# Performance work log

Hardware: AMD Instinct MI355X
Metric: run time of the kernel (lower is better)

## Reference

```python
import jax, jax.numpy as jnp
import numpy as np

N_NODES = 50000
N_EDGES = 800000
IN_DIM = 128
HID = 128
N_LAYERS = 3
MASK_RATE = 0.3
NUM_MASK = int(MASK_RATE * N_NODES)  # 15000


def setup_inputs() -> dict:
    key = jax.random.key(0)
    ks = jax.random.split(key, 8)
    attr = jax.random.normal(ks[0], (N_NODES, IN_DIM), dtype=jnp.float32)
    src = jax.random.randint(ks[1], (N_EDGES,), 0, N_NODES, dtype=jnp.int32)
    dst = jax.random.randint(ks[2], (N_EDGES,), 0, N_NODES, dtype=jnp.int32)
    # GraphConv weights (glorot-ish scale)
    Ws = jax.random.normal(ks[3], (N_LAYERS, HID, HID), dtype=jnp.float32) * (1.0 / np.sqrt(HID))
    bs = jnp.zeros((N_LAYERS, HID), dtype=jnp.float32)
    dec_W = jax.random.normal(ks[4], (HID, IN_DIM), dtype=jnp.float32) * (1.0 / np.sqrt(HID))
    dec_b = jnp.zeros((IN_DIM,), dtype=jnp.float32)
    mask_token = jnp.zeros((1, IN_DIM), dtype=jnp.float32)
    # torch.randperm(N)[:num_mask]
    perm = jax.random.permutation(ks[5], N_NODES)
    mask_nodes = perm[:NUM_MASK].astype(jnp.int32)
    return {"attr": attr, "src": src, "dst": dst, "Ws": Ws, "bs": bs,
            "dec_W": dec_W, "dec_b": dec_b, "mask_token": mask_token,
            "mask_nodes": mask_nodes}


def reference(attr, src, dst, Ws, bs, dec_W, dec_b, mask_token, mask_nodes):
    # degree norms (DGL GraphConv norm='both'), zero-degree clamped to 1
    ones = jnp.ones((src.shape[0],), dtype=jnp.float32)
    out_deg = jax.ops.segment_sum(ones, src, num_segments=N_NODES)
    in_deg = jax.ops.segment_sum(ones, dst, num_segments=N_NODES)
    norm_src = jnp.power(jnp.clip(out_deg, 1.0, None), -0.5)[:, None]  # [N,1]
    norm_dst = jnp.power(jnp.clip(in_deg, 1.0, None), -0.5)[:, None]

    # mask node features with the mask token
    h = attr.at[mask_nodes].set(mask_token[0])

    for i in range(N_LAYERS):
        h = h @ Ws[i]                       # [N, H]
        m = (h * norm_src)[src]             # gather: [E, H]
        agg = jax.ops.segment_sum(m, dst, num_segments=N_NODES)
        h = jax.nn.relu(agg * norm_dst + bs[i])

    recon = h @ dec_W + dec_b               # [N, IN_DIM]
    x_orig = attr[mask_nodes]
    x_rec = recon[mask_nodes]
    loss = jnp.mean((x_rec - x_orig) ** 2)
    return loss
```

## Files before the change

### kernel.cpp

```cpp
#include <hip/hip_runtime.h>
#include <hip/hip_fp16.h>

#define HID 128
#define NN 50000
#define NW4 (NN / 4)
#define NB 256
#define CST 64

typedef _Float16 f16;
typedef f16 f16x8 __attribute__((ext_vector_type(8)));
typedef float f32x4 __attribute__((ext_vector_type(4)));

__device__ __forceinline__ unsigned char enc8(float v) {
  __half h = __float2half(v);
  unsigned short b;
  __builtin_memcpy(&b, &h, 2);
  return (unsigned char)((b + 0x80u) >> 8);
}
__device__ __forceinline__ __half2 dec8h2(unsigned v) {
  unsigned p = __builtin_amdgcn_perm(0u, v, 0x01040004u);
  __half2 h2;
  __builtin_memcpy(&h2, &p, 4);
  return h2;
}
__device__ __forceinline__ f16x8 dec8x8(const unsigned char* p) {
  uint2 u = *(const uint2*)p;
  unsigned r[4];
  r[0] = __builtin_amdgcn_perm(0u, u.x, 0x01040004u);
  r[1] = __builtin_amdgcn_perm(0u, u.x, 0x03040204u);
  r[2] = __builtin_amdgcn_perm(0u, u.y, 0x01040004u);
  r[3] = __builtin_amdgcn_perm(0u, u.y, 0x03040204u);
  f16x8 out;
  __builtin_memcpy(&out, r, 16);
  return out;
}

__global__ __launch_bounds__(256) void hist_kernel(
    const int* __restrict__ src, const int* __restrict__ dst,
    unsigned* __restrict__ pin, unsigned* __restrict__ pout,
    unsigned char* __restrict__ rank, float* __restrict__ d_out_f,
    unsigned* __restrict__ mmap_w, int E, int chunk) {
  __shared__ unsigned hist[NW4];
  const int b = blockIdx.x;
  const int e0 = b * chunk, e1 = min(E, e0 + chunk);
  if (b == 0 && threadIdx.x == 0) *d_out_f = 0.f;
  if (b < 49) {
    int wi = b * 256 + threadIdx.x;
    if (wi < NW4) mmap_w[wi] = 0;
  }

  for (int i = threadIdx.x; i < NW4; i += 256) hist[i] = 0;
  __syncthreads();
  for (int e = e0 + threadIdx.x; e < e1; e += 256) {
    int d = dst[e];
    unsigned sh = 8u * (d & 3);
    unsigned old = atomicAdd(&hist[d >> 2], 1u << sh);
    rank[e] = (unsigned char)((old >> sh) & 0xffu);
  }
  __syncthreads();
  unsigned* rowI = pin + (size_t)b * NW4;
  for (int i = threadIdx.x; i < NW4; i += 256) rowI[i] = hist[i];
  __syncthreads();
  for (int i = threadIdx.x; i < NW4; i += 256) hist[i] = 0;
  __syncthreads();
  for (int e = e0 + threadIdx.x; e < e1; e += 256) {
    int s = src[e];
    atomicAdd(&hist[s >> 2], 1u << (8u * (s & 3)));
  }
  __syncthreads();
  unsigned* rowO = pout + (size_t)b * NW4;
  for (int i = threadIdx.x; i < NW4; i += 256) rowO[i] = hist[i];
}

__global__ __launch_bounds__(256) void merge_kernel(
    unsigned* __restrict__ pin, const unsigned* __restrict__ pout,
    int* __restrict__ in_cnt, float* __restrict__ ns, float* __restrict__ nd,
    const int* __restrict__ mask, unsigned char* __restrict__ mmap, int nm) {
  int gi = blockIdx.x * 256 + threadIdx.x;
  if (gi < nm) mmap[mask[gi]] = 1;

  __shared__ unsigned tsum[8][32];
  __shared__ unsigned osum[8][32];
  const int wl = threadIdx.x & 31;
  const int tile = threadIdx.x >> 5;
  const int w = blockIdx.x * 32 + wl;
  const bool ok = w < NW4;

  unsigned v[32];
  unsigned s = 0, so = 0;
  if (ok) {
#pragma unroll
    for (int j = 0; j < 32; ++j)
      v[j] = pin[(size_t)(tile * 32 + j) * NW4 + w];
#pragma unroll
    for (int j = 0; j < 32; ++j) {
      unsigned x = v[j];
      v[j] = s;
      s += x;
    }
#pragma unroll
    for (int j = 0; j < 32; ++j)
      so += pout[(size_t)(tile * 32 + j) * NW4 + w];
  }
  tsum[tile][wl] = s;
  osum[tile][wl] = so;
  __syncthreads();
  unsigned toff = 0;
  for (int k = 0; k < tile; ++k) toff += tsum[k][wl];
  if (ok) {
#pragma unroll
    for (int j = 0; j < 32; ++j)
      pin[(size_t)(tile * 32 + j) * NW4 + w] = v[j] + toff;
    if (tile == 7) {
      unsigned tin = toff + s;
      unsigned tout = 0;
#pragma unroll
      for (int k = 0; k < 8; ++k) tout += osum[k][wl];
      int i0 = tin & 0xffu, i1 = (tin >> 8) & 0xffu,
          i2 = (tin >> 16) & 0xffu, i3 = (tin >> 24) & 0xffu;
      int o0 = tout & 0xffu, o1 = (tout >> 8) & 0xffu,
          o2 = (tout >> 16) & 0xffu, o3 = (tout >> 24) & 0xffu;
      ((int4*)in_cnt)[w] = make_int4(i0, i1, i2, i3);
      ((float4*)nd)[w] = make_float4(rsqrtf((float)max(i0, 1)),
                                     rsqrtf((float)max(i1, 1)),
                                     rsqrtf((float)max(i2, 1)),
                                     rsqrtf((float)max(i3, 1)));
      ((float4*)ns)[w] = make_float4(rsqrtf((float)max(o0, 1)),
                                     rsqrtf((float)max(o1, 1)),
                                     rsqrtf((float)max(o2, 1)),
                                     rsqrtf((float)max(o3, 1)));
    }
  }
}

__global__ __launch_bounds__(256) void fillprep_kernel(
    const int* __restrict__ src, const int* __restrict__ dst,
    const unsigned char* __restrict__ rank, const unsigned* __restrict__ pin,
    int* __restrict__ csr,
    const float* __restrict__ attr, const float* __restrict__ Ws,
    const float* __restrict__ decW, const float* __restrict__ ns,
    const float* __restrict__ token, const unsigned char* __restrict__ mmap,
    unsigned char* __restrict__ X, f16* __restrict__ Wt,
    int E, int chunk, int n4) {
  const int b = blockIdx.x;
  if (b < 256) {
    const int e0 = b * chunk, e1 = min(E, e0 + chunk);
    const unsigned* __restrict__ row = pin + (size_t)b * NW4;
    for (int e = e0 + threadIdx.x; e < e1; e += 256) {
      int s = src[e], d = dst[e];
      unsigned base = (row[d >> 2] >> (8u * (d & 3))) & 0xffu;
      csr[d * CST + (int)base + (int)rank[e]] = s;
    }
  } else if (b < 512) {
    int i = (b - 256) * 256 + threadIdx.x;
    int m = i >> 14, rem = i & 16383, n = rem >> 7, k = rem & 127;
    const float* Wsrc = (m < 3) ? (Ws + (size_t)m * 16384) : decW;
    Wt[i] = (f16)Wsrc[k * 128 + n];
  } else {
    int i = (b - 512) * 256 + threadIdx.x;
    if (i < n4) {
      int r = i >> 5, c4 = i & 31;
      float s = ns[r];
      float4 v = mmap[r] ? ((const float4*)token)[c4] : ((const float4*)attr)[i];
      ((uchar4*)X)[i] = make_uchar4(enc8(s * v.x), enc8(s * v.y),
                                    enc8(s * v.z), enc8(s * v.w));
    }
  }
}

__global__ __launch_bounds__(256) void agg_kernel(
    const unsigned short* __restrict__ X, const int* __restrict__ csr,
    const int* __restrict__ in_cnt, const float* __restrict__ nd,
    const int* __restrict__ glist, unsigned short* __restrict__ Y, int n) {
  int ni = (blockIdx.x * blockDim.x + threadIdx.x) >> 6;
  int lane = threadIdx.x & 63;
  if (ni >= n) return;
  int node = glist ? glist[ni] : ni;
  int cnt = in_cnt[node];
  int idx = csr[node * CST + lane];
  __half2 z = __floats2half2_rn(0.f, 0.f);
  __half2 a0 = z, a1 = z, a2 = z, a3 = z;
  int i = 0;
  for (; i + 4 <= cnt; i += 4) {
    int s0 = __shfl(idx, i + 0);
    int s1 = __shfl(idx, i + 1);
    int s2 = __shfl(idx, i + 2);
    int s3 = __shfl(idx, i + 3);
    __half2 v0 = dec8h2(X[(size_t)s0 * 64 + lane]);
    __half2 v1 = dec8h2(X[(size_t)s1 * 64 + lane]);
    __half2 v2 = dec8h2(X[(size_t)s2 * 64 + lane]);
    __half2 v3 = dec8h2(X[(size_t)s3 * 64 + lane]);
    a0 = __hadd2(a0, v0);
    a1 = __hadd2(a1, v1);
    a2 = __hadd2(a2, v2);
    a3 = __hadd2(a3, v3);
  }
  for (; i < cnt; ++i) {
    int s = __shfl(idx, i);
    a0 = __hadd2(a0, dec8h2(X[(size_t)s * 64 + lane]));
  }
  __half2 hs = __hadd2(__hadd2(a0, a1), __hadd2(a2, a3));
  float2 f = __half22float2(hs);
  float ndv = nd[node];
  unsigned char lo = enc8(f.x * ndv), hi = enc8(f.y * ndv);
  Y[(size_t)ni * 64 + lane] = (unsigned short)(lo | (hi << 8));
}

__global__ __launch_bounds__(256) void gemm_layer_kernel(
    const unsigned char* __restrict__ A8, const f16* __restrict__ Wt,
    unsigned char* __restrict__ out, const float* __restrict__ col_bias,
    const float* __restrict__ row_scale, int M) {
  __shared__ f16 Bs[128 * 136];
  const int t = threadIdx.x;
  for (int i = t; i < 2048; i += 256) {
    int n = i >> 4, c = i & 15;
    *(f16x8*)&Bs[n * 136 + c * 8] = *(const f16x8*)&Wt[n * 128 + c * 8];
  }
  const int wave = t >> 6, lane = t & 63;
  const int ln = lane & 15, kq = lane >> 4;
  const int mBase = blockIdx.x * 64 + wave * 16;

  const int am = mBase + ln;
  const int rowA = (am < M) ? am : 0;
  const unsigned char* Ap = A8 + (size_t)rowA * HID + kq * 8;
  f16x8 af[4];
#pragma unroll
  for (int ki = 0; ki < 4; ++ki) af[ki] = dec8x8(Ap + ki * 32);

  f32x4 acc[8];
#pragma unroll
  for (int nt = 0; nt < 8; ++nt) acc[nt] = (f32x4){0.f, 0.f, 0.f, 0.f};
  __syncthreads();
#pragma unroll
  for (int ki = 0; ki < 4; ++ki) {
#pragma unroll
    for (int nt = 0; nt < 8; ++nt) {
      f16x8 bf = *(const f16x8*)&Bs[(nt * 16 + ln) * 136 + ki * 32 + kq * 8];
      acc[nt] = __builtin_amdgcn_mfma_f32_16x16x32_f16(af[ki], bf, acc[nt], 0, 0, 0);
    }
  }
  const int orow = mBase + kq * 4;
  float rs[4];
#pragma unroll
  for (int r = 0; r < 4; ++r)
    rs[r] = (row_scale && orow + r < M) ? row_scale[orow + r] : 1.f;
#pragma unroll
  for (int nt = 0; nt < 8; ++nt) {
    int col = nt * 16 + ln;
    float bb = col_bias[col];
#pragma unroll
    for (int r = 0; r < 4; ++r) {
      int gr = orow + r;
      if (gr < M) {
        float v = fmaxf(acc[nt][r] + bb, 0.f) * rs[r];
        out[(size_t)gr * HID + col] = enc8(v);
      }
    }
  }
}

__global__ __launch_bounds__(256) void gemm_loss_kernel(
    const unsigned char* __restrict__ A8, const f16* __restrict__ Wt,
    const float* __restrict__ col_bias, const int* __restrict__ mask,
    const float* __restrict__ attr, float* __restrict__ out, int M, float scale) {
  __shared__ f16 Bs[128 * 136];
  const int t = threadIdx.x;
  for (int i = t; i < 2048; i += 256) {
    int n = i >> 4, c = i & 15;
    *(f16x8*)&Bs[n * 136 + c * 8] = *(const f16x8*)&Wt[n * 128 + c * 8];
  }
  const int wave = t >> 6, lane = t & 63;
  const int ln = lane & 15, kq = lane >> 4;
  const int mBase = blockIdx.x * 64 + wave * 16;

  const int am = mBase + ln;
  const int rowA = (am < M) ? am : 0;
  const unsigned char* Ap = A8 + (size_t)rowA * HID + kq * 8;
  f16x8 af[4];
#pragma unroll
  for (int ki = 0; ki < 4; ++ki) af[ki] = dec8x8(Ap + ki * 32);

  f32x4 acc[8];
#pragma unroll
  for (int nt = 0; nt < 8; ++nt) acc[nt] = (f32x4){0.f, 0.f, 0.f, 0.f};
  __syncthreads();
#pragma unroll
  for (int ki = 0; ki < 4; ++ki) {
#pragma unroll
    for (int nt = 0; nt < 8; ++nt) {
      f16x8 bf = *(const f16x8*)&Bs[(nt * 16 + ln) * 136 + ki * 32 + kq * 8];
      acc[nt] = __builtin_amdgcn_mfma_f32_16x16x32_f16(af[ki], bf, acc[nt], 0, 0, 0);
    }
  }
  const int orow = mBase + kq * 4;
  int mrow[4];
#pragma unroll
  for (int r = 0; r < 4; ++r) mrow[r] = (orow + r < M) ? mask[orow + r] : -1;
  float part = 0.f;
#pragma unroll
  for (int nt = 0; nt < 8; ++nt) {
    int col = nt * 16 + ln;
    float bb = col_bias[col];
#pragma unroll
    for (int r = 0; r < 4; ++r) {
      if (mrow[r] >= 0) {
        float d = acc[nt][r] + bb - attr[(size_t)mrow[r] * HID + col];
        part += d * d;
      }
    }
  }
#pragma unroll
  for (int off = 32; off > 0; off >>= 1) part += __shfl_down(part, off);
  __shared__ float wsum[4];
  if (lane == 0) wsum[wave] = part;
  __syncthreads();
  if (t == 0)
    atomicAdd(out, (wsum[0] + wsum[1] + wsum[2] + wsum[3]) * scale);
}

extern "C" void kernel_launch(void* const* d_in, const int* in_sizes, int n_in,
                              void* d_out, int out_size, void* d_ws, size_t ws_size,
                              hipStream_t stream) {
  const float* attr  = (const float*)d_in[0];
  const int*   src   = (const int*)d_in[1];
  const int*   dst   = (const int*)d_in[2];
  const float* Ws    = (const float*)d_in[3];
  const float* bs    = (const float*)d_in[4];
  const float* decW  = (const float*)d_in[5];
  const float* decb  = (const float*)d_in[6];
  const float* token = (const float*)d_in[7];
  const int*   mask  = (const int*)d_in[8];

  const int N  = in_sizes[0] / HID;
  const int E  = in_sizes[1];
  const int NM = in_sizes[8];
  const int chunk = (E + NB - 1) / NB;

  char* w = (char*)d_ws;
  unsigned char* X = (unsigned char*)w;  w += (size_t)N * HID;
  unsigned char* Y = (unsigned char*)w;  w += (size_t)N * HID;
  f16* Wt = (f16*)w;           w += (size_t)4 * HID * HID * 2;
  int* csr = (int*)w;          w += (size_t)NN * CST * 4;
  unsigned char* rank = (unsigned char*)w;  w += (size_t)E;
  unsigned* pin = (unsigned*)w;  w += (size_t)NB * NW4 * 4;
  unsigned* pout = (unsigned*)w; w += (size_t)NB * NW4 * 4;
  int* in_cnt = (int*)w;       w += (size_t)N * 4;
  float* ns = (float*)w;       w += (size_t)N * 4;
  float* nd = (float*)w;       w += (size_t)N * 4;
  unsigned char* mmap = (unsigned char*)w;  w += (size_t)NW4 * 4;

  hist_kernel<<<NB, 256, 0, stream>>>(src, dst, pin, pout, rank,
                                      (float*)d_out, (unsigned*)mmap, E, chunk);
  merge_kernel<<<(NW4 + 31) / 32, 256, 0, stream>>>(pin, pout, in_cnt, ns, nd,
                                                    mask, mmap, NM);

  int prep_blocks = 512 + (N * 32 + 255) / 256;
  fillprep_kernel<<<prep_blocks, 256, 0, stream>>>(
      src, dst, rank, pin, csr, attr, Ws, decW, ns, token, mmap,
      X, Wt, E, chunk, N * 32);

  for (int l = 0; l < 2; ++l) {
    agg_kernel<<<(N + 3) / 4, 256, 0, stream>>>(
        (const unsigned short*)X, csr, in_cnt, nd, nullptr,
        (unsigned short*)Y, N);
    gemm_layer_kernel<<<(N + 63) / 64, 256, 0, stream>>>(
        Y, Wt + (size_t)l * HID * HID, X, bs + (size_t)l * HID, ns, N);
  }

  agg_kernel<<<(NM + 3) / 4, 256, 0, stream>>>(
      (const unsigned short*)X, csr, in_cnt, nd, mask,
      (unsigned short*)Y, NM);
  gemm_layer_kernel<<<(NM + 63) / 64, 256, 0, stream>>>(
      Y, Wt + (size_t)2 * HID * HID, X, bs + (size_t)2 * HID, nullptr, NM);

  gemm_loss_kernel<<<(NM + 63) / 64, 256, 0, stream>>>(
      X, Wt + (size_t)3 * HID * HID, decb, mask, attr, (float*)d_out,
      NM, 1.f / ((float)NM * HID));
}
```

Before: 239.5 us.

## Replace deterministic histogram CSR build with global atomic bucket fill

Replaces the three-kernel build (per-block shared-memory histograms, a prefix-merge kernel, and a separate fill pass) with one edge-parallel kernel. It uses global atomics on the in-degree counters to claim CSR slots and atomics on out-degree, and zeroes the counters with a memset. Degree norms are no longer stored; they are recomputed with rsqrt from the integer counts wherever they are used. This removes two launches and the large partial-histogram traffic, but global atomic contention costs more and neighbor order inside the CSR becomes nondeterministic, which can change the fp16 summation order.

```diff
diff --git a/kernel.cpp b/kernel.cpp
--- a/kernel.cpp
+++ b/kernel.cpp
@@ -3,8 +3,6 @@
 
 #define HID 128
 #define NN 50000
-#define NW4 (NN / 4)
-#define NB 256
 #define CST 64
 
 typedef _Float16 f16;
@@ -35,132 +33,38 @@
   return out;
 }
 
-__global__ __launch_bounds__(256) void hist_kernel(
+__global__ __launch_bounds__(256) void build_kernel(
     const int* __restrict__ src, const int* __restrict__ dst,
-    unsigned* __restrict__ pin, unsigned* __restrict__ pout,
-    unsigned char* __restrict__ rank, float* __restrict__ d_out_f,
-    unsigned* __restrict__ mmap_w, int E, int chunk) {
-  __shared__ unsigned hist[NW4];
-  const int b = blockIdx.x;
-  const int e0 = b * chunk, e1 = min(E, e0 + chunk);
-  if (b == 0 && threadIdx.x == 0) *d_out_f = 0.f;
-  if (b < 49) {
-    int wi = b * 256 + threadIdx.x;
-    if (wi < NW4) mmap_w[wi] = 0;
-  }
-
-  for (int i = threadIdx.x; i < NW4; i += 256) hist[i] = 0;
-  __syncthreads();
-  for (int e = e0 + threadIdx.x; e < e1; e += 256) {
-    int d = dst[e];
-    unsigned sh = 8u * (d & 3);
-    unsigned old = atomicAdd(&hist[d >> 2], 1u << sh);
-    rank[e] = (unsigned char)((old >> sh) & 0xffu);
-  }
-  __syncthreads();
-  unsigned* rowI = pin + (size_t)b * NW4;
-  for (int i = threadIdx.x; i < NW4; i += 256) rowI[i] = hist[i];
-  __syncthreads();
-  for (int i = threadIdx.x; i < NW4; i += 256) hist[i] = 0;
-  __syncthreads();
-  for (int e = e0 + threadIdx.x; e < e1; e += 256) {
-    int s = src[e];
-    atomicAdd(&hist[s >> 2], 1u << (8u * (s & 3)));
-  }
-  __syncthreads();
-  unsigned* rowO = pout + (size_t)b * NW4;
-  for (int i = threadIdx.x; i < NW4; i += 256) rowO[i] = hist[i];
-}
-
-__global__ __launch_bounds__(256) void merge_kernel(
-    unsigned* __restrict__ pin, const unsigned* __restrict__ pout,
-    int* __restrict__ in_cnt, float* __restrict__ ns, float* __restrict__ nd,
-    const int* __restrict__ mask, unsigned char* __restrict__ mmap, int nm) {
+    int* __restrict__ cin, int* __restrict__ odeg,
+    int* __restrict__ csr,
+    const int* __restrict__ mask, unsigned char* __restrict__ mmap,
+    int E, int nm) {
   int gi = blockIdx.x * 256 + threadIdx.x;
   if (gi < nm) mmap[mask[gi]] = 1;
-
-  __shared__ unsigned tsum[8][32];
-  __shared__ unsigned osum[8][32];
-  const int wl = threadIdx.x & 31;
-  const int tile = threadIdx.x >> 5;
-  const int w = blockIdx.x * 32 + wl;
-  const bool ok = w < NW4;
-
-  unsigned v[32];
-  unsigned s = 0, so = 0;
-  if (ok) {
-#pragma unroll
-    for (int j = 0; j < 32; ++j)
-      v[j] = pin[(size_t)(tile * 32 + j) * NW4 + w];
-#pragma unroll
-    for (int j = 0; j < 32; ++j) {
-      unsigned x = v[j];
-      v[j] = s;
-      s += x;
-    }
-#pragma unroll
-    for (int j = 0; j < 32; ++j)
-      so += pout[(size_t)(tile * 32 + j) * NW4 + w];
-  }
-  tsum[tile][wl] = s;
-  osum[tile][wl] = so;
-  __syncthreads();
-  unsigned toff = 0;
-  for (int k = 0; k < tile; ++k) toff += tsum[k][wl];
-  if (ok) {
-#pragma unroll
-    for (int j = 0; j < 32; ++j)
-      pin[(size_t)(tile * 32 + j) * NW4 + w] = v[j] + toff;
-    if (tile == 7) {
-      unsigned tin = toff + s;
-      unsigned tout = 0;
-#pragma unroll
-      for (int k = 0; k < 8; ++k) tout += osum[k][wl];
-      int i0 = tin & 0xffu, i1 = (tin >> 8) & 0xffu,
-          i2 = (tin >> 16) & 0xffu, i3 = (tin >> 24) & 0xffu;
-      int o0 = tout & 0xffu, o1 = (tout >> 8) & 0xffu,
-          o2 = (tout >> 16) & 0xffu, o3 = (tout >> 24) & 0xffu;
-      ((int4*)in_cnt)[w] = make_int4(i0, i1, i2, i3);
-      ((float4*)nd)[w] = make_float4(rsqrtf((float)max(i0, 1)),
-                                     rsqrtf((float)max(i1, 1)),
-                                     rsqrtf((float)max(i2, 1)),
-                                     rsqrtf((float)max(i3, 1)));
-      ((float4*)ns)[w] = make_float4(rsqrtf((float)max(o0, 1)),
-                                     rsqrtf((float)max(o1, 1)),
-                                     rsqrtf((float)max(o2, 1)),
-                                     rsqrtf((float)max(o3, 1)));
-    }
-  }
-}
-
-__global__ __launch_bounds__(256) void fillprep_kernel(
-    const int* __restrict__ src, const int* __restrict__ dst,
-    const unsigned char* __restrict__ rank, const unsigned* __restrict__ pin,
-    int* __restrict__ csr,
+  if (gi < E) {
+    int s = src[gi], d = dst[gi];
+    int r = atomicAdd(&cin[d], 1);
+    csr[d * CST + r] = s;
+    atomicAdd(&odeg[s], 1);
+  }
+}
+
+__global__ __launch_bounds__(256) void prep_kernel(
     const float* __restrict__ attr, const float* __restrict__ Ws,
-    const float* __restrict__ decW, const float* __restrict__ ns,
+    const float* __restrict__ decW, const int* __restrict__ odeg,
     const float* __restrict__ token, const unsigned char* __restrict__ mmap,
-    unsigned char* __restrict__ X, f16* __restrict__ Wt,
-    int E, int chunk, int n4) {
+    unsigned char* __restrict__ X, f16* __restrict__ Wt, int n4) {
   const int b = blockIdx.x;
   if (b < 256) {
-    const int e0 = b * chunk, e1 = min(E, e0 + chunk);
-    const unsigned* __restrict__ row = pin + (size_t)b * NW4;
-    for (int e = e0 + threadIdx.x; e < e1; e += 256) {
-      int s = src[e], d = dst[e];
-      unsigned base = (row[d >> 2] >> (8u * (d & 3))) & 0xffu;
-      csr[d * CST + (int)base + (int)rank[e]] = s;
-    }
-  } else if (b < 512) {
-    int i = (b - 256) * 256 + threadIdx.x;
+    int i = b * 256 + threadIdx.x;
     int m = i >> 14, rem = i & 16383, n = rem >> 7, k = rem & 127;
     const float* Wsrc = (m < 3) ? (Ws + (size_t)m * 16384) : decW;
     Wt[i] = (f16)Wsrc[k * 128 + n];
   } else {
-    int i = (b - 512) * 256 + threadIdx.x;
+    int i = (b - 256) * 256 + threadIdx.x;
     if (i < n4) {
       int r = i >> 5, c4 = i & 31;
-      float s = ns[r];
+      float s = rsqrtf((float)max(odeg[r], 1));
       float4 v = mmap[r] ? ((const float4*)token)[c4] : ((const float4*)attr)[i];
       ((uchar4*)X)[i] = make_uchar4(enc8(s * v.x), enc8(s * v.y),
                                     enc8(s * v.z), enc8(s * v.w));
@@ -170,8 +74,8 @@
 
 __global__ __launch_bounds__(256) void agg_kernel(
     const unsigned short* __restrict__ X, const int* __restrict__ csr,
-    const int* __restrict__ in_cnt, const float* __restrict__ nd,
-    const int* __restrict__ glist, unsigned short* __restrict__ Y, int n) {
+    const int* __restrict__ in_cnt, const int* __restrict__ glist,
+    unsigned short* __restrict__ Y, int n) {
   int ni = (blockIdx.x * blockDim.x + threadIdx.x) >> 6;
   int lane = threadIdx.x & 63;
   if (ni >= n) return;
@@ -201,7 +105,7 @@
   }
   __half2 hs = __hadd2(__hadd2(a0, a1), __hadd2(a2, a3));
   float2 f = __half22float2(hs);
-  float ndv = nd[node];
+  float ndv = rsqrtf((float)max(cnt, 1));
   unsigned char lo = enc8(f.x * ndv), hi = enc8(f.y * ndv);
   Y[(size_t)ni * 64 + lane] = (unsigned short)(lo | (hi << 8));
 }
@@ -209,7 +113,7 @@
 __global__ __launch_bounds__(256) void gemm_layer_kernel(
     const unsigned char* __restrict__ A8, const f16* __restrict__ Wt,
     unsigned char* __restrict__ out, const float* __restrict__ col_bias,
-    const float* __restrict__ row_scale, int M) {
+    const int* __restrict__ row_deg, int M) {
   __shared__ f16 Bs[128 * 136];
   const int t = threadIdx.x;
   for (int i = t; i < 2048; i += 256) {
@@ -243,7 +147,8 @@
   float rs[4];
 #pragma unroll
   for (int r = 0; r < 4; ++r)
-    rs[r] = (row_scale && orow + r < M) ? row_scale[orow + r] : 1.f;
+    rs[r] = (row_deg && orow + r < M) ? rsqrtf((float)max(row_deg[orow + r], 1))
+                                      : 1.f;
 #pragma unroll
   for (int nt = 0; nt < 8; ++nt) {
     int col = nt * 16 + ln;
@@ -334,41 +239,36 @@
   const int N  = in_sizes[0] / HID;
   const int E  = in_sizes[1];
   const int NM = in_sizes[8];
-  const int chunk = (E + NB - 1) / NB;
 
   char* w = (char*)d_ws;
   unsigned char* X = (unsigned char*)w;  w += (size_t)N * HID;
   unsigned char* Y = (unsigned char*)w;  w += (size_t)N * HID;
   f16* Wt = (f16*)w;           w += (size_t)4 * HID * HID * 2;
   int* csr = (int*)w;          w += (size_t)NN * CST * 4;
-  unsigned char* rank = (unsigned char*)w;  w += (size_t)E;
-  unsigned* pin = (unsigned*)w;  w += (size_t)NB * NW4 * 4;
-  unsigned* pout = (unsigned*)w; w += (size_t)NB * NW4 * 4;
-  int* in_cnt = (int*)w;       w += (size_t)N * 4;
-  float* ns = (float*)w;       w += (size_t)N * 4;
-  float* nd = (float*)w;       w += (size_t)N * 4;
-  unsigned char* mmap = (unsigned char*)w;  w += (size_t)NW4 * 4;
-
-  hist_kernel<<<NB, 256, 0, stream>>>(src, dst, pin, pout, rank,
-                                      (float*)d_out, (unsigned*)mmap, E, chunk);
-  merge_kernel<<<(NW4 + 31) / 32, 256, 0, stream>>>(pin, pout, in_cnt, ns, nd,
-                                                    mask, mmap, NM);
-
-  int prep_blocks = 512 + (N * 32 + 255) / 256;
-  fillprep_kernel<<<prep_blocks, 256, 0, stream>>>(
-      src, dst, rank, pin, csr, attr, Ws, decW, ns, token, mmap,
-      X, Wt, E, chunk, N * 32);
+  int* cin = (int*)w;          w += (size_t)N * 4;
+  int* odeg = (int*)w;         w += (size_t)N * 4;
+  unsigned char* mmap = (unsigned char*)w;  w += (size_t)N;
+
+  hipMemsetAsync(cin, 0, (size_t)N * 8 + (size_t)N, stream);
+  hipMemsetAsync(d_out, 0, sizeof(float), stream);
+
+  build_kernel<<<(E + 255) / 256, 256, 0, stream>>>(
+      src, dst, cin, odeg, csr, mask, mmap, E, NM);
+
+  int prep_blocks = 256 + (N * 32 + 255) / 256;
+  prep_kernel<<<prep_blocks, 256, 0, stream>>>(
+      attr, Ws, decW, odeg, token, mmap, X, Wt, N * 32);
 
   for (int l = 0; l < 2; ++l) {
     agg_kernel<<<(N + 3) / 4, 256, 0, stream>>>(
-        (const unsigned short*)X, csr, in_cnt, nd, nullptr,
+        (const unsigned short*)X, csr, cin, nullptr,
         (unsigned short*)Y, N);
     gemm_layer_kernel<<<(N + 63) / 64, 256, 0, stream>>>(
-        Y, Wt + (size_t)l * HID * HID, X, bs + (size_t)l * HID, ns, N);
+        Y, Wt + (size_t)l * HID * HID, X, bs + (size_t)l * HID, odeg, N);
   }
 
   agg_kernel<<<(NM + 3) / 4, 256, 0, stream>>>(
-      (const unsigned short*)X, csr, in_cnt, nd, mask,
+      (const unsigned short*)X, csr, cin, mask,
       (unsigned short*)Y, NM);
   gemm_layer_kernel<<<(NM + 63) / 64, 256, 0, stream>>>(
       Y, Wt + (size_t)2 * HID * HID, X, bs + (size_t)2 * HID, nullptr, NM);
```

New measurement: 272.6 us. +13.8%, slower.

## Fuse neighbor aggregation into GEMM kernels and merge last layer with decoder loss

Applied to the files above, without the earlier changes.

Aggregation now runs inside the GEMM kernels: each wave gathers 16 rows into shared memory as fp16, with the next row's CSR prefetched and the gather loop unrolled 8-wide. The final layer, decoder GEMM and loss are fused into one kernel. This drops the Y intermediate round-trip through global memory and several launches, and computes norm_dst with rsqrtf instead of a load. It also vectorizes the histogram clears and copies with uint4. The cost is that one wave now serially aggregates 16 nodes, which lowers gather parallelism per block and raises shared memory use and register pressure.

```diff
diff --git a/kernel.cpp b/kernel.cpp
--- a/kernel.cpp
+++ b/kernel.cpp
@@ -22,17 +22,6 @@
   __half2 h2;
   __builtin_memcpy(&h2, &p, 4);
   return h2;
-}
-__device__ __forceinline__ f16x8 dec8x8(const unsigned char* p) {
-  uint2 u = *(const uint2*)p;
-  unsigned r[4];
-  r[0] = __builtin_amdgcn_perm(0u, u.x, 0x01040004u);
-  r[1] = __builtin_amdgcn_perm(0u, u.x, 0x03040204u);
-  r[2] = __builtin_amdgcn_perm(0u, u.y, 0x01040004u);
-  r[3] = __builtin_amdgcn_perm(0u, u.y, 0x03040204u);
-  f16x8 out;
-  __builtin_memcpy(&out, r, 16);
-  return out;
 }
 
 __global__ __launch_bounds__(256) void hist_kernel(
@@ -49,7 +38,8 @@
     if (wi < NW4) mmap_w[wi] = 0;
   }
 
-  for (int i = threadIdx.x; i < NW4; i += 256) hist[i] = 0;
+  uint4* h4 = (uint4*)hist;
+  for (int i = threadIdx.x; i < NW4 / 4; i += 256) h4[i] = make_uint4(0, 0, 0, 0);
   __syncthreads();
   for (int e = e0 + threadIdx.x; e < e1; e += 256) {
     int d = dst[e];
@@ -58,18 +48,18 @@
     rank[e] = (unsigned char)((old >> sh) & 0xffu);
   }
   __syncthreads();
-  unsigned* rowI = pin + (size_t)b * NW4;
-  for (int i = threadIdx.x; i < NW4; i += 256) rowI[i] = hist[i];
-  __syncthreads();
-  for (int i = threadIdx.x; i < NW4; i += 256) hist[i] = 0;
+  uint4* rowI = (uint4*)(pin + (size_t)b * NW4);
+  for (int i = threadIdx.x; i < NW4 / 4; i += 256) rowI[i] = h4[i];
+  __syncthreads();
+  for (int i = threadIdx.x; i < NW4 / 4; i += 256) h4[i] = make_uint4(0, 0, 0, 0);
   __syncthreads();
   for (int e = e0 + threadIdx.x; e < e1; e += 256) {
     int s = src[e];
     atomicAdd(&hist[s >> 2], 1u << (8u * (s & 3)));
   }
   __syncthreads();
-  unsigned* rowO = pout + (size_t)b * NW4;
-  for (int i = threadIdx.x; i < NW4; i += 256) rowO[i] = hist[i];
+  uint4* rowO = (uint4*)(pout + (size_t)b * NW4);
+  for (int i = threadIdx.x; i < NW4 / 4; i += 256) rowO[i] = h4[i];
 }
 
 __global__ __launch_bounds__(256) void merge_kernel(
@@ -168,69 +158,84 @@
   }
 }
 
-__global__ __launch_bounds__(256) void agg_kernel(
-    const unsigned short* __restrict__ X, const int* __restrict__ csr,
-    const int* __restrict__ in_cnt, const float* __restrict__ nd,
-    const int* __restrict__ glist, unsigned short* __restrict__ Y, int n) {
-  int ni = (blockIdx.x * blockDim.x + threadIdx.x) >> 6;
-  int lane = threadIdx.x & 63;
-  if (ni >= n) return;
-  int node = glist ? glist[ni] : ni;
-  int cnt = in_cnt[node];
-  int idx = csr[node * CST + lane];
-  __half2 z = __floats2half2_rn(0.f, 0.f);
-  __half2 a0 = z, a1 = z, a2 = z, a3 = z;
-  int i = 0;
-  for (; i + 4 <= cnt; i += 4) {
-    int s0 = __shfl(idx, i + 0);
-    int s1 = __shfl(idx, i + 1);
-    int s2 = __shfl(idx, i + 2);
-    int s3 = __shfl(idx, i + 3);
-    __half2 v0 = dec8h2(X[(size_t)s0 * 64 + lane]);
-    __half2 v1 = dec8h2(X[(size_t)s1 * 64 + lane]);
-    __half2 v2 = dec8h2(X[(size_t)s2 * 64 + lane]);
-    __half2 v3 = dec8h2(X[(size_t)s3 * 64 + lane]);
-    a0 = __hadd2(a0, v0);
-    a1 = __hadd2(a1, v1);
-    a2 = __hadd2(a2, v2);
-    a3 = __hadd2(a3, v3);
-  }
-  for (; i < cnt; ++i) {
-    int s = __shfl(idx, i);
-    a0 = __hadd2(a0, dec8h2(X[(size_t)s * 64 + lane]));
-  }
-  __half2 hs = __hadd2(__hadd2(a0, a1), __hadd2(a2, a3));
-  float2 f = __half22float2(hs);
-  float ndv = nd[node];
-  unsigned char lo = enc8(f.x * ndv), hi = enc8(f.y * ndv);
-  Y[(size_t)ni * 64 + lane] = (unsigned short)(lo | (hi << 8));
-}
-
-__global__ __launch_bounds__(256) void gemm_layer_kernel(
-    const unsigned char* __restrict__ A8, const f16* __restrict__ Wt,
-    unsigned char* __restrict__ out, const float* __restrict__ col_bias,
-    const float* __restrict__ row_scale, int M) {
+template <bool USE_GLIST>
+__device__ __forceinline__ void agg16(
+    const unsigned short* __restrict__ Xin, const int* __restrict__ csr,
+    const int* __restrict__ in_cnt, const int* __restrict__ glist,
+    int mBase, int wave, int lane, int M, f16* __restrict__ Ar) {
+  int cnt = 0, idx = 0;
+  if (mBase < M) {
+    int node = USE_GLIST ? glist[mBase] : mBase;
+    cnt = in_cnt[node];
+    idx = csr[node * CST + lane];
+  }
+  const __half2 z = __floats2half2_rn(0.f, 0.f);
+  for (int j = 0; j < 16; ++j) {
+    int cnt_n = 0, idx_n = 0;
+    int row1 = mBase + j + 1;
+    if (j < 15 && row1 < M) {
+      int node1 = USE_GLIST ? glist[row1] : row1;
+      cnt_n = in_cnt[node1];
+      idx_n = csr[node1 * CST + lane];
+    }
+    __half2 a0 = z, a1 = z, a2 = z, a3 = z, a4 = z, a5 = z, a6 = z, a7 = z;
+    int i = 0;
+    for (; i + 8 <= cnt; i += 8) {
+      int s0 = __shfl(idx, i + 0), s1 = __shfl(idx, i + 1);
+      int s2 = __shfl(idx, i + 2), s3 = __shfl(idx, i + 3);
+      int s4 = __shfl(idx, i + 4), s5 = __shfl(idx, i + 5);
+      int s6 = __shfl(idx, i + 6), s7 = __shfl(idx, i + 7);
+      a0 = __hadd2(a0, dec8h2(Xin[(size_t)s0 * 64 + lane]));
+      a1 = __hadd2(a1, dec8h2(Xin[(size_t)s1 * 64 + lane]));
+      a2 = __hadd2(a2, dec8h2(Xin[(size_t)s2 * 64 + lane]));
+      a3 = __hadd2(a3, dec8h2(Xin[(size_t)s3 * 64 + lane]));
+      a4 = __hadd2(a4, dec8h2(Xin[(size_t)s4 * 64 + lane]));
+      a5 = __hadd2(a5, dec8h2(Xin[(size_t)s5 * 64 + lane]));
+      a6 = __hadd2(a6, dec8h2(Xin[(size_t)s6 * 64 + lane]));
+      a7 = __hadd2(a7, dec8h2(Xin[(size_t)s7 * 64 + lane]));
+    }
+    for (; i < cnt; ++i) {
+      int s = __shfl(idx, i);
+      a0 = __hadd2(a0, dec8h2(Xin[(size_t)s * 64 + lane]));
+    }
+    __half2 hs = __hadd2(__hadd2(__hadd2(a0, a1), __hadd2(a2, a3)),
+                         __hadd2(__hadd2(a4, a5), __hadd2(a6, a7)));
+    float2 f = __half22float2(hs);
+    float ndv = rsqrtf((float)max(cnt, 1));
+    *(__half2*)&Ar[(wave * 16 + j) * 136 + 2 * lane] =
+        __floats2half2_rn(f.x * ndv, f.y * ndv);
+    cnt = cnt_n;
+    idx = idx_n;
+  }
+}
+
+__global__ __launch_bounds__(256) void ag_layer_kernel(
+    const unsigned short* __restrict__ Xin, const int* __restrict__ csr,
+    const int* __restrict__ in_cnt, const f16* __restrict__ Wt,
+    const float* __restrict__ col_bias, const float* __restrict__ ns,
+    unsigned char* __restrict__ Xout, int M) {
   __shared__ f16 Bs[128 * 136];
+  __shared__ f16 Ar[64 * 136];
   const int t = threadIdx.x;
   for (int i = t; i < 2048; i += 256) {
     int n = i >> 4, c = i & 15;
     *(f16x8*)&Bs[n * 136 + c * 8] = *(const f16x8*)&Wt[n * 128 + c * 8];
   }
   const int wave = t >> 6, lane = t & 63;
+  const int mBase = blockIdx.x * 64 + wave * 16;
+
+  agg16<false>(Xin, csr, in_cnt, nullptr, mBase, wave, lane, M, Ar);
+  __syncthreads();
+
   const int ln = lane & 15, kq = lane >> 4;
-  const int mBase = blockIdx.x * 64 + wave * 16;
-
-  const int am = mBase + ln;
-  const int rowA = (am < M) ? am : 0;
-  const unsigned char* Ap = A8 + (size_t)rowA * HID + kq * 8;
   f16x8 af[4];
 #pragma unroll
-  for (int ki = 0; ki < 4; ++ki) af[ki] = dec8x8(Ap + ki * 32);
+  for (int ki = 0; ki < 4; ++ki)
+    af[ki] = *(const f16x8*)&Ar[(wave * 16 + ln) * 136 + ki * 32 + kq * 8];
 
   f32x4 acc[8];
 #pragma unroll
   for (int nt = 0; nt < 8; ++nt) acc[nt] = (f32x4){0.f, 0.f, 0.f, 0.f};
-  __syncthreads();
 #pragma unroll
   for (int ki = 0; ki < 4; ++ki) {
 #pragma unroll
@@ -243,7 +248,7 @@
   float rs[4];
 #pragma unroll
   for (int r = 0; r < 4; ++r)
-    rs[r] = (row_scale && orow + r < M) ? row_scale[orow + r] : 1.f;
+    rs[r] = (orow + r < M) ? ns[orow + r] : 1.f;
 #pragma unroll
   for (int nt = 0; nt < 8; ++nt) {
     int col = nt * 16 + ln;
@@ -253,37 +258,43 @@
       int gr = orow + r;
       if (gr < M) {
         float v = fmaxf(acc[nt][r] + bb, 0.f) * rs[r];
-        out[(size_t)gr * HID + col] = enc8(v);
+        Xout[(size_t)gr * HID + col] = enc8(v);
       }
     }
   }
 }
 
-__global__ __launch_bounds__(256) void gemm_loss_kernel(
-    const unsigned char* __restrict__ A8, const f16* __restrict__ Wt,
-    const float* __restrict__ col_bias, const int* __restrict__ mask,
-    const float* __restrict__ attr, float* __restrict__ out, int M, float scale) {
+__global__ __launch_bounds__(256) void ag_loss_kernel(
+    const unsigned short* __restrict__ Xin, const int* __restrict__ csr,
+    const int* __restrict__ in_cnt, const f16* __restrict__ W2t,
+    const f16* __restrict__ Dt, const float* __restrict__ b2,
+    const float* __restrict__ decb, const int* __restrict__ mask,
+    const float* __restrict__ attr, float* __restrict__ out,
+    int M, float scale) {
   __shared__ f16 Bs[128 * 136];
+  __shared__ f16 Ds[128 * 136];
+  __shared__ f16 Ar[64 * 136];
   const int t = threadIdx.x;
   for (int i = t; i < 2048; i += 256) {
     int n = i >> 4, c = i & 15;
-    *(f16x8*)&Bs[n * 136 + c * 8] = *(const f16x8*)&Wt[n * 128 + c * 8];
+    *(f16x8*)&Bs[n * 136 + c * 8] = *(const f16x8*)&W2t[n * 128 + c * 8];
+    *(f16x8*)&Ds[n * 136 + c * 8] = *(const f16x8*)&Dt[n * 128 + c * 8];
   }
   const int wave = t >> 6, lane = t & 63;
+  const int mBase = blockIdx.x * 64 + wave * 16;
+
+  agg16<true>(Xin, csr, in_cnt, mask, mBase, wave, lane, M, Ar);
+  __syncthreads();
+
   const int ln = lane & 15, kq = lane >> 4;
-  const int mBase = blockIdx.x * 64 + wave * 16;
-
-  const int am = mBase + ln;
-  const int rowA = (am < M) ? am : 0;
-  const unsigned char* Ap = A8 + (size_t)rowA * HID + kq * 8;
   f16x8 af[4];
 #pragma unroll
-  for (int ki = 0; ki < 4; ++ki) af[ki] = dec8x8(Ap + ki * 32);
+  for (int ki = 0; ki < 4; ++ki)
+    af[ki] = *(const f16x8*)&Ar[(wave * 16 + ln) * 136 + ki * 32 + kq * 8];
 
   f32x4 acc[8];
 #pragma unroll
   for (int nt = 0; nt < 8; ++nt) acc[nt] = (f32x4){0.f, 0.f, 0.f, 0.f};
-  __syncthreads();
 #pragma unroll
   for (int ki = 0; ki < 4; ++ki) {
 #pragma unroll
@@ -293,6 +304,31 @@
     }
   }
   const int orow = mBase + kq * 4;
+#pragma unroll
+  for (int nt = 0; nt < 8; ++nt) {
+    int col = nt * 16 + ln;
+    float bb = b2[col];
+#pragma unroll
+    for (int r = 0; r < 4; ++r) {
+      float v = fmaxf(acc[nt][r] + bb, 0.f);
+      Ar[(wave * 16 + kq * 4 + r) * 136 + col] = (f16)v;
+    }
+  }
+  __syncthreads();
+
+#pragma unroll
+  for (int ki = 0; ki < 4; ++ki)
+    af[ki] = *(const f16x8*)&Ar[(wave * 16 + ln) * 136 + ki * 32 + kq * 8];
+#pragma unroll
+  for (int nt = 0; nt < 8; ++nt) acc[nt] = (f32x4){0.f, 0.f, 0.f, 0.f};
+#pragma unroll
+  for (int ki = 0; ki < 4; ++ki) {
+#pragma unroll
+    for (int nt = 0; nt < 8; ++nt) {
+      f16x8 bf = *(const f16x8*)&Ds[(nt * 16 + ln) * 136 + ki * 32 + kq * 8];
+      acc[nt] = __builtin_amdgcn_mfma_f32_16x16x32_f16(af[ki], bf, acc[nt], 0, 0, 0);
+    }
+  }
   int mrow[4];
 #pragma unroll
   for (int r = 0; r < 4; ++r) mrow[r] = (orow + r < M) ? mask[orow + r] : -1;
@@ -300,7 +336,7 @@
 #pragma unroll
   for (int nt = 0; nt < 8; ++nt) {
     int col = nt * 16 + ln;
-    float bb = col_bias[col];
+    float bb = decb[col];
 #pragma unroll
     for (int r = 0; r < 4; ++r) {
       if (mrow[r] >= 0) {
@@ -337,8 +373,8 @@
   const int chunk = (E + NB - 1) / NB;
 
   char* w = (char*)d_ws;
-  unsigned char* X = (unsigned char*)w;  w += (size_t)N * HID;
-  unsigned char* Y = (unsigned char*)w;  w += (size_t)N * HID;
+  unsigned char* XA = (unsigned char*)w;  w += (size_t)N * HID;
+  unsigned char* XB = (unsigned char*)w;  w += (size_t)N * HID;
   f16* Wt = (f16*)w;           w += (size_t)4 * HID * HID * 2;
   int* csr = (int*)w;          w += (size_t)NN * CST * 4;
   unsigned char* rank = (unsigned char*)w;  w += (size_t)E;
@@ -357,23 +393,17 @@
   int prep_blocks = 512 + (N * 32 + 255) / 256;
   fillprep_kernel<<<prep_blocks, 256, 0, stream>>>(
       src, dst, rank, pin, csr, attr, Ws, decW, ns, token, mmap,
-      X, Wt, E, chunk, N * 32);
-
-  for (int l = 0; l < 2; ++l) {
-    agg_kernel<<<(N + 3) / 4, 256, 0, stream>>>(
-        (const unsigned short*)X, csr, in_cnt, nd, nullptr,
-        (unsigned short*)Y, N);
-    gemm_layer_kernel<<<(N + 63) / 64, 256, 0, stream>>>(
-        Y, Wt + (size_t)l * HID * HID, X, bs + (size_t)l * HID, ns, N);
-  }
-
-  agg_kernel<<<(NM + 3) / 4, 256, 0, stream>>>(
-      (const unsigned short*)X, csr, in_cnt, nd, mask,
-      (unsigned short*)Y, NM);
-  gemm_layer_kernel<<<(NM + 63) / 64, 256, 0, stream>>>(
-      Y, Wt + (size_t)2 * HID * HID, X, bs + (size_t)2 * HID, nullptr, NM);
-
-  gemm_loss_kernel<<<(NM + 63) / 64, 256, 0, stream>>>(
-      X, Wt + (size_t)3 * HID * HID, decb, mask, attr, (float*)d_out,
+      XA, Wt, E, chunk, N * 32);
+
+  ag_layer_kernel<<<(N + 63) / 64, 256, 0, stream>>>(
+      (const unsigned short*)XA, csr, in_cnt, Wt, bs, ns, XB, N);
+  ag_layer_kernel<<<(N + 63) / 64, 256, 0, stream>>>(
+      (const unsigned short*)XB, csr, in_cnt, Wt + (size_t)HID * HID,
+      bs + HID, ns, XA, N);
+
+  ag_loss_kernel<<<(NM + 63) / 64, 256, 0, stream>>>(
+      (const unsigned short*)XA, csr, in_cnt,
+      Wt + (size_t)2 * HID * HID, Wt + (size_t)3 * HID * HID,
+      bs + 2 * HID, decb, mask, attr, (float*)d_out,
       NM, 1.f / ((float)NM * HID));
 }
```

Result: slower. 349.7 us (+46.0%).

## Fuse last layer GEMM with decoder loss, widen agg gathers, vectorize histogram copies

Applied to the files above, without the earlier changes.

The final layer GEMM (bias plus ReLU) is fused into the decoder/loss kernel. The intermediate activations stay in shared memory as fp16 instead of being round-tripped through global memory as 8-bit, which also removes one launch. The aggregation kernel now loads 4-byte words with half-waves handling alternate neighbors, then combines the halves with an xor-32 shuffle. It also computes the in-degree norm inline rather than reading a precomputed array. Histogram zeroing and copy-out use uint4 stores. The fused kernel needs extra LDS (about 86KB per block), which may limit occupancy.

```diff
diff --git a/kernel.cpp b/kernel.cpp
--- a/kernel.cpp
+++ b/kernel.cpp
@@ -17,8 +17,14 @@
   __builtin_memcpy(&b, &h, 2);
   return (unsigned char)((b + 0x80u) >> 8);
 }
-__device__ __forceinline__ __half2 dec8h2(unsigned v) {
+__device__ __forceinline__ __half2 dec8lo(unsigned v) {
   unsigned p = __builtin_amdgcn_perm(0u, v, 0x01040004u);
+  __half2 h2;
+  __builtin_memcpy(&h2, &p, 4);
+  return h2;
+}
+__device__ __forceinline__ __half2 dec8hi(unsigned v) {
+  unsigned p = __builtin_amdgcn_perm(0u, v, 0x03040204u);
   __half2 h2;
   __builtin_memcpy(&h2, &p, 4);
   return h2;
@@ -33,6 +39,14 @@
   f16x8 out;
   __builtin_memcpy(&out, r, 16);
   return out;
+}
+__device__ __forceinline__ __half2 xor32_add(__half2 v) {
+  int b;
+  __builtin_memcpy(&b, &v, 4);
+  int g = __shfl_xor(b, 32);
+  __half2 w;
+  __builtin_memcpy(&w, &g, 4);
+  return __hadd2(v, w);
 }
 
 __global__ __launch_bounds__(256) void hist_kernel(
@@ -49,7 +63,8 @@
     if (wi < NW4) mmap_w[wi] = 0;
   }
 
-  for (int i = threadIdx.x; i < NW4; i += 256) hist[i] = 0;
+  uint4* h4 = (uint4*)hist;
+  for (int i = threadIdx.x; i < NW4 / 4; i += 256) h4[i] = make_uint4(0, 0, 0, 0);
   __syncthreads();
   for (int e = e0 + threadIdx.x; e < e1; e += 256) {
     int d = dst[e];
@@ -58,23 +73,23 @@
     rank[e] = (unsigned char)((old >> sh) & 0xffu);
   }
   __syncthreads();
-  unsigned* rowI = pin + (size_t)b * NW4;
-  for (int i = threadIdx.x; i < NW4; i += 256) rowI[i] = hist[i];
-  __syncthreads();
-  for (int i = threadIdx.x; i < NW4; i += 256) hist[i] = 0;
+  uint4* rowI = (uint4*)(pin + (size_t)b * NW4);
+  for (int i = threadIdx.x; i < NW4 / 4; i += 256) rowI[i] = h4[i];
+  __syncthreads();
+  for (int i = threadIdx.x; i < NW4 / 4; i += 256) h4[i] = make_uint4(0, 0, 0, 0);
   __syncthreads();
   for (int e = e0 + threadIdx.x; e < e1; e += 256) {
     int s = src[e];
     atomicAdd(&hist[s >> 2], 1u << (8u * (s & 3)));
   }
   __syncthreads();
-  unsigned* rowO = pout + (size_t)b * NW4;
-  for (int i = threadIdx.x; i < NW4; i += 256) rowO[i] = hist[i];
+  uint4* rowO = (uint4*)(pout + (size_t)b * NW4);
+  for (int i = threadIdx.x; i < NW4 / 4; i += 256) rowO[i] = h4[i];
 }
 
 __global__ __launch_bounds__(256) void merge_kernel(
     unsigned* __restrict__ pin, const unsigned* __restrict__ pout,
-    int* __restrict__ in_cnt, float* __restrict__ ns, float* __restrict__ nd,
+    int* __restrict__ in_cnt, float* __restrict__ ns,
     const int* __restrict__ mask, unsigned char* __restrict__ mmap, int nm) {
   int gi = blockIdx.x * 256 + threadIdx.x;
   if (gi < nm) mmap[mask[gi]] = 1;
@@ -121,10 +136,6 @@
       int o0 = tout & 0xffu, o1 = (tout >> 8) & 0xffu,
           o2 = (tout >> 16) & 0xffu, o3 = (tout >> 24) & 0xffu;
       ((int4*)in_cnt)[w] = make_int4(i0, i1, i2, i3);
-      ((float4*)nd)[w] = make_float4(rsqrtf((float)max(i0, 1)),
-                                     rsqrtf((float)max(i1, 1)),
-                                     rsqrtf((float)max(i2, 1)),
-                                     rsqrtf((float)max(i3, 1)));
       ((float4*)ns)[w] = make_float4(rsqrtf((float)max(o0, 1)),
                                      rsqrtf((float)max(o1, 1)),
                                      rsqrtf((float)max(o2, 1)),
@@ -169,41 +180,65 @@
 }
 
 __global__ __launch_bounds__(256) void agg_kernel(
-    const unsigned short* __restrict__ X, const int* __restrict__ csr,
-    const int* __restrict__ in_cnt, const float* __restrict__ nd,
-    const int* __restrict__ glist, unsigned short* __restrict__ Y, int n) {
+    const unsigned* __restrict__ Xw, const int* __restrict__ csr,
+    const int* __restrict__ in_cnt, const int* __restrict__ glist,
+    unsigned* __restrict__ Y, int n) {
   int ni = (blockIdx.x * blockDim.x + threadIdx.x) >> 6;
   int lane = threadIdx.x & 63;
   if (ni >= n) return;
   int node = glist ? glist[ni] : ni;
   int cnt = in_cnt[node];
   int idx = csr[node * CST + lane];
-  __half2 z = __floats2half2_rn(0.f, 0.f);
-  __half2 a0 = z, a1 = z, a2 = z, a3 = z;
+  const int half = lane >> 5, sub = lane & 31;
+  const __half2 z = __floats2half2_rn(0.f, 0.f);
+  __half2 a00 = z, a01 = z, a10 = z, a11 = z;
+  __half2 a20 = z, a21 = z, a30 = z, a31 = z;
   int i = 0;
-  for (; i + 4 <= cnt; i += 4) {
-    int s0 = __shfl(idx, i + 0);
-    int s1 = __shfl(idx, i + 1);
-    int s2 = __shfl(idx, i + 2);
-    int s3 = __shfl(idx, i + 3);
-    __half2 v0 = dec8h2(X[(size_t)s0 * 64 + lane]);
-    __half2 v1 = dec8h2(X[(size_t)s1 * 64 + lane]);
-    __half2 v2 = dec8h2(X[(size_t)s2 * 64 + lane]);
-    __half2 v3 = dec8h2(X[(size_t)s3 * 64 + lane]);
-    a0 = __hadd2(a0, v0);
-    a1 = __hadd2(a1, v1);
-    a2 = __hadd2(a2, v2);
-    a3 = __hadd2(a3, v3);
-  }
-  for (; i < cnt; ++i) {
+  for (; i + 8 <= cnt; i += 8) {
+    int s0 = __shfl(idx, i + 0 + half);
+    int s1 = __shfl(idx, i + 2 + half);
+    int s2 = __shfl(idx, i + 4 + half);
+    int s3 = __shfl(idx, i + 6 + half);
+    unsigned u0 = Xw[(size_t)s0 * 32 + sub];
+    unsigned u1 = Xw[(size_t)s1 * 32 + sub];
+    unsigned u2 = Xw[(size_t)s2 * 32 + sub];
+    unsigned u3 = Xw[(size_t)s3 * 32 + sub];
+    a00 = __hadd2(a00, dec8lo(u0));
+    a01 = __hadd2(a01, dec8hi(u0));
+    a10 = __hadd2(a10, dec8lo(u1));
+    a11 = __hadd2(a11, dec8hi(u1));
+    a20 = __hadd2(a20, dec8lo(u2));
+    a21 = __hadd2(a21, dec8hi(u2));
+    a30 = __hadd2(a30, dec8lo(u3));
+    a31 = __hadd2(a31, dec8hi(u3));
+  }
+  for (; i + 2 <= cnt; i += 2) {
+    int s = __shfl(idx, i + half);
+    unsigned u = Xw[(size_t)s * 32 + sub];
+    a00 = __hadd2(a00, dec8lo(u));
+    a01 = __hadd2(a01, dec8hi(u));
+  }
+  if (i < cnt) {
     int s = __shfl(idx, i);
-    a0 = __hadd2(a0, dec8h2(X[(size_t)s * 64 + lane]));
-  }
-  __half2 hs = __hadd2(__hadd2(a0, a1), __hadd2(a2, a3));
-  float2 f = __half22float2(hs);
-  float ndv = nd[node];
-  unsigned char lo = enc8(f.x * ndv), hi = enc8(f.y * ndv);
-  Y[(size_t)ni * 64 + lane] = (unsigned short)(lo | (hi << 8));
+    unsigned u = Xw[(size_t)s * 32 + sub];
+    if (half) u = 0;
+    a00 = __hadd2(a00, dec8lo(u));
+    a01 = __hadd2(a01, dec8hi(u));
+  }
+  __half2 s0 = __hadd2(__hadd2(a00, a10), __hadd2(a20, a30));
+  __half2 s1 = __hadd2(__hadd2(a01, a11), __hadd2(a21, a31));
+  s0 = xor32_add(s0);
+  s1 = xor32_add(s1);
+  float ndv = rsqrtf((float)max(cnt, 1));
+  float2 f0 = __half22float2(s0);
+  float2 f1 = __half22float2(s1);
+  if (half == 0) {
+    unsigned pack = (unsigned)enc8(f0.x * ndv) |
+                    ((unsigned)enc8(f0.y * ndv) << 8) |
+                    ((unsigned)enc8(f1.x * ndv) << 16) |
+                    ((unsigned)enc8(f1.y * ndv) << 24);
+    Y[(size_t)ni * 32 + sub] = pack;
+  }
 }
 
 __global__ __launch_bounds__(256) void gemm_layer_kernel(
@@ -259,15 +294,20 @@
   }
 }
 
-__global__ __launch_bounds__(256) void gemm_loss_kernel(
-    const unsigned char* __restrict__ A8, const f16* __restrict__ Wt,
-    const float* __restrict__ col_bias, const int* __restrict__ mask,
-    const float* __restrict__ attr, float* __restrict__ out, int M, float scale) {
+__global__ __launch_bounds__(256) void gemm2_loss_kernel(
+    const unsigned char* __restrict__ A8, const f16* __restrict__ W2t,
+    const f16* __restrict__ Dt, const float* __restrict__ b2,
+    const float* __restrict__ decb, const int* __restrict__ mask,
+    const float* __restrict__ attr, float* __restrict__ out,
+    int M, float scale) {
   __shared__ f16 Bs[128 * 136];
+  __shared__ f16 Ds[128 * 136];
+  __shared__ f16 Ar[64 * 136];
   const int t = threadIdx.x;
   for (int i = t; i < 2048; i += 256) {
     int n = i >> 4, c = i & 15;
-    *(f16x8*)&Bs[n * 136 + c * 8] = *(const f16x8*)&Wt[n * 128 + c * 8];
+    *(f16x8*)&Bs[n * 136 + c * 8] = *(const f16x8*)&W2t[n * 128 + c * 8];
+    *(f16x8*)&Ds[n * 136 + c * 8] = *(const f16x8*)&Dt[n * 128 + c * 8];
   }
   const int wave = t >> 6, lane = t & 63;
   const int ln = lane & 15, kq = lane >> 4;
@@ -293,6 +333,31 @@
     }
   }
   const int orow = mBase + kq * 4;
+#pragma unroll
+  for (int nt = 0; nt < 8; ++nt) {
+    int col = nt * 16 + ln;
+    float bb = b2[col];
+#pragma unroll
+    for (int r = 0; r < 4; ++r) {
+      float v = fmaxf(acc[nt][r] + bb, 0.f);
+      Ar[(wave * 16 + kq * 4 + r) * 136 + col] = (f16)v;
+    }
+  }
+  __syncthreads();
+
+#pragma unroll
+  for (int ki = 0; ki < 4; ++ki)
+    af[ki] = *(const f16x8*)&Ar[(wave * 16 + ln) * 136 + ki * 32 + kq * 8];
+#pragma unroll
+  for (int nt = 0; nt < 8; ++nt) acc[nt] = (f32x4){0.f, 0.f, 0.f, 0.f};
+#pragma unroll
+  for (int ki = 0; ki < 4; ++ki) {
+#pragma unroll
+    for (int nt = 0; nt < 8; ++nt) {
+      f16x8 bf = *(const f16x8*)&Ds[(nt * 16 + ln) * 136 + ki * 32 + kq * 8];
+      acc[nt] = __builtin_amdgcn_mfma_f32_16x16x32_f16(af[ki], bf, acc[nt], 0, 0, 0);
+    }
+  }
   int mrow[4];
 #pragma unroll
   for (int r = 0; r < 4; ++r) mrow[r] = (orow + r < M) ? mask[orow + r] : -1;
@@ -300,7 +365,7 @@
 #pragma unroll
   for (int nt = 0; nt < 8; ++nt) {
     int col = nt * 16 + ln;
-    float bb = col_bias[col];
+    float bb = decb[col];
 #pragma unroll
     for (int r = 0; r < 4; ++r) {
       if (mrow[r] >= 0) {
@@ -346,12 +411,11 @@
   unsigned* pout = (unsigned*)w; w += (size_t)NB * NW4 * 4;
   int* in_cnt = (int*)w;       w += (size_t)N * 4;
   float* ns = (float*)w;       w += (size_t)N * 4;
-  float* nd = (float*)w;       w += (size_t)N * 4;
   unsigned char* mmap = (unsigned char*)w;  w += (size_t)NW4 * 4;
 
   hist_kernel<<<NB, 256, 0, stream>>>(src, dst, pin, pout, rank,
                                       (float*)d_out, (unsigned*)mmap, E, chunk);
-  merge_kernel<<<(NW4 + 31) / 32, 256, 0, stream>>>(pin, pout, in_cnt, ns, nd,
+  merge_kernel<<<(NW4 + 31) / 32, 256, 0, stream>>>(pin, pout, in_cnt, ns,
                                                     mask, mmap, NM);
 
   int prep_blocks = 512 + (N * 32 + 255) / 256;
@@ -361,19 +425,16 @@
 
   for (int l = 0; l < 2; ++l) {
     agg_kernel<<<(N + 3) / 4, 256, 0, stream>>>(
-        (const unsigned short*)X, csr, in_cnt, nd, nullptr,
-        (unsigned short*)Y, N);
+        (const unsigned*)X, csr, in_cnt, nullptr, (unsigned*)Y, N);
     gemm_layer_kernel<<<(N + 63) / 64, 256, 0, stream>>>(
         Y, Wt + (size_t)l * HID * HID, X, bs + (size_t)l * HID, ns, N);
   }
 
   agg_kernel<<<(NM + 3) / 4, 256, 0, stream>>>(
-      (const unsigned short*)X, csr, in_cnt, nd, mask,
-      (unsigned short*)Y, NM);
-  gemm_layer_kernel<<<(NM + 63) / 64, 256, 0, stream>>>(
-      Y, Wt + (size_t)2 * HID * HID, X, bs + (size_t)2 * HID, nullptr, NM);
-
-  gemm_loss_kernel<<<(NM + 63) / 64, 256, 0, stream>>>(
-      X, Wt + (size_t)3 * HID * HID, decb, mask, attr, (float*)d_out,
+      (const unsigned*)X, csr, in_cnt, mask, (unsigned*)Y, NM);
+
+  gemm2_loss_kernel<<<(NM + 63) / 64, 256, 0, stream>>>(
+      Y, Wt + (size_t)2 * HID * HID, Wt + (size_t)3 * HID * HID,
+      bs + 2 * HID, decb, mask, attr, (float*)d_out,
       NM, 1.f / ((float)NM * HID));
 }
```

Measured after the change: 218.9 us. 1.09x faster.
